# Kernel tuning notes

Hardware: AMD Instinct MI355X
Metric: run time of the kernel (lower is better)

## Reference

```python
import jax, jax.numpy as jnp
import numpy as np

N_NODES = 50000
N_EDGES = 800000
C_IN = 128
C_OUT = 128
K = 6


def setup_inputs() -> dict:
    key = jax.random.key(0)
    ks = jax.random.split(key, 8)
    nodes = jax.random.normal(ks[0], (N_NODES, C_IN), dtype=jnp.float32)
    edges = jax.random.uniform(ks[1], (N_EDGES,), dtype=jnp.float32)
    senders = jax.random.randint(ks[2], (N_EDGES,), 0, N_NODES, dtype=jnp.int32)
    receivers = jax.random.randint(ks[3], (N_EDGES,), 0, N_NODES, dtype=jnp.int32)
    # K independent Dense(out_channels) layers (kernel + bias each), plus extra module bias
    W = jax.random.normal(ks[4], (K, C_IN, C_OUT), dtype=jnp.float32) / jnp.sqrt(jnp.float32(C_IN))
    b_dense = jax.random.normal(ks[5], (K, C_OUT), dtype=jnp.float32) * 0.01
    bias = jnp.zeros((C_OUT,), dtype=jnp.float32)
    return {"nodes": nodes, "edges": edges, "senders": senders, "receivers": receivers,
            "W": W, "b_dense": b_dense, "bias": bias}


def reference(nodes, edges, senders, receivers, W, b_dense, bias):
    n = nodes.shape[0]
    # Laplacian L = D - A with A[s, r] = w. deg_i = sum of weights of edges with sender i.
    deg = jax.ops.segment_sum(edges, senders, num_segments=n)
    # lambda_max = 2 * max(L.data) where L.data = concat(deg, -edges)
    lambda_max = 2.0 * jnp.maximum(deg.max(), (-edges).max())
    scale = 2.0 / lambda_max  # L_hat = (2/lambda_max) * L

    def Lmatvec(x):  # (2L/lambda_max) @ x via gather + segment_sum
        agg = jax.ops.segment_sum(edges[:, None] * x[receivers], senders, num_segments=n)
        return scale * (deg[:, None] * x - agg)

    Tx0 = nodes
    out = Tx0 @ W[0] + b_dense[0]
    Tx1 = Lmatvec(Tx0)
    out = out + Tx1 @ W[1] + b_dense[1]
    for k in range(2, K):
        Tx2 = 2.0 * Lmatvec(Tx1) - Tx0
        out = out + Tx2 @ W[k] + b_dense[k]
        Tx0, Tx1 = Tx1, Tx2
    return out + bias
```

## Files before the change

kernel.cpp:

```cpp
#include <hip/hip_runtime.h>

#define C 128
#define KORD 6
#define KD (KORD * C)
#define EPB 2048

typedef __attribute__((ext_vector_type(8))) short short8;
typedef __attribute__((ext_vector_type(4))) float f32x4;

__device__ __forceinline__ short f2bf(float f) {
  unsigned u = __float_as_uint(f);
  unsigned r = (u + 0x7fffu + ((u >> 16) & 1u)) >> 16;
  return (short)r;
}
__device__ __forceinline__ float bf2f(short s) {
  return __uint_as_float(((unsigned)(unsigned short)s) << 16);
}

__device__ __forceinline__ unsigned enc_f32(float f) {
  unsigned u = __float_as_uint(f);
  return (u & 0x80000000u) ? ~u : (u | 0x80000000u);
}
__device__ __forceinline__ float dec_f32(unsigned u) {
  return (u & 0x80000000u) ? __uint_as_float(u ^ 0x80000000u) : __uint_as_float(~u);
}

__global__ void prep_kernel(const float* __restrict__ W, const float* __restrict__ bd,
                            const float* __restrict__ bias, short* __restrict__ Wt,
                            float* __restrict__ bsum, const float* __restrict__ nodes,
                            short* __restrict__ xb, int n) {
  int i = blockIdx.x * blockDim.x + threadIdx.x;
  if (i < KD * C) {
    int k = i >> 7, nn = i & 127;
    Wt[(size_t)nn * KD + k] = f2bf(W[i]);
  }
  if (i < C) {
    float s = bias[i];
#pragma unroll
    for (int k = 0; k < KORD; ++k) s += bd[k * C + i];
    bsum[i] = s;
  }
  if (i < n * 32) {
    int row = i >> 5, c4 = i & 31;
    float4 v = ((const float4*)nodes)[(size_t)row * 32 + c4];
    short4 o;
    o.x = f2bf(v.x); o.y = f2bf(v.y); o.z = f2bf(v.z); o.w = f2bf(v.w);
    ((short4*)(xb + (size_t)row * KD))[c4] = o;
  }
}

__global__ __launch_bounds__(256) void p1_count_kernel(const int* __restrict__ senders,
                                                       const float* __restrict__ edges, int ne,
                                                       int* __restrict__ hist, int NB,
                                                       unsigned* __restrict__ umax) {
  __shared__ int h[256];
  int t = threadIdx.x;
  h[t] = 0;
  __syncthreads();
  int base = blockIdx.x * EPB;
  int end = min(base + EPB, ne);
  float m = -INFINITY;
  for (int i = base + t; i < end; i += 256) {
    atomicAdd(&h[senders[i] >> 8], 1);
    m = fmaxf(m, -edges[i]);
  }
#pragma unroll
  for (int off = 32; off > 0; off >>= 1) m = fmaxf(m, __shfl_down(m, off, 64));
  if ((t & 63) == 0) atomicMax(umax, enc_f32(m));
  __syncthreads();
  hist[t * NB + blockIdx.x] = h[t];
}

__global__ __launch_bounds__(1024) void scan1_kernel(const int* __restrict__ counts,
                                                     int* __restrict__ offsets,
                                                     int* __restrict__ bsums, int n) {
  int t = threadIdx.x;
  int i = blockIdx.x * 1024 + t;
  int lane = t & 63, w = t >> 6;
  int v = (i < n) ? counts[i] : 0;
  int s = v;
#pragma unroll
  for (int d = 1; d < 64; d <<= 1) {
    int o = __shfl_up(s, d, 64);
    if (lane >= d) s += o;
  }
  __shared__ int wsum[16];
  if (lane == 63) wsum[w] = s;
  __syncthreads();
  if (t < 16) {
    int ws = wsum[t];
#pragma unroll
    for (int d = 1; d < 16; d <<= 1) {
      int o = __shfl_up(ws, d, 64);
      if (t >= d) ws += o;
    }
    wsum[t] = ws;
  }
  __syncthreads();
  int excl = s - v + (w > 0 ? wsum[w - 1] : 0);
  if (i < n) offsets[i] = excl;
  if (t == 1023) bsums[blockIdx.x] = wsum[15];
}

__global__ __launch_bounds__(1024) void scan2_kernel(int* __restrict__ bsums, int nb) {
  int t = threadIdx.x;
  int lane = t & 63, w = t >> 6;
  int v = (t < nb) ? bsums[t] : 0;
  int s = v;
#pragma unroll
  for (int d = 1; d < 64; d <<= 1) {
    int o = __shfl_up(s, d, 64);
    if (lane >= d) s += o;
  }
  __shared__ int wsum[16];
  if (lane == 63) wsum[w] = s;
  __syncthreads();
  if (t < 16) {
    int ws = wsum[t];
#pragma unroll
    for (int d = 1; d < 16; d <<= 1) {
      int o = __shfl_up(ws, d, 64);
      if (t >= d) ws += o;
    }
    wsum[t] = ws;
  }
  __syncthreads();
  int excl = s - v + (w > 0 ? wsum[w - 1] : 0);
  if (t < nb) bsums[t] = excl;
}

__global__ __launch_bounds__(256) void p1_scatter_kernel(
    const int* __restrict__ senders, const int* __restrict__ receivers,
    const float* __restrict__ edges, int ne, const int* __restrict__ scanned,
    const int* __restrict__ bsums, int NB, int2* __restrict__ bkt) {
  __shared__ int basec[256];
  int t = threadIdx.x;
  int idx = t * NB + blockIdx.x;
  basec[t] = scanned[idx] + bsums[idx >> 10];
  __syncthreads();
  int base = blockIdx.x * EPB;
  int end = min(base + EPB, ne);
  for (int i = base + t; i < end; i += 256) {
    int s = senders[i];
    int pos = atomicAdd(&basec[s >> 8], 1);
    int2 rec;
    rec.x = __float_as_int(edges[i]);
    rec.y = receivers[i] | ((s & 255) << 16);
    bkt[pos] = rec;
  }
}

__global__ __launch_bounds__(256) void p2_finalize_kernel(
    const int2* __restrict__ bkt, const int* __restrict__ scanned,
    const int* __restrict__ bsums, int NB, int NBUCK, int ne, int n, int2* __restrict__ csr_wr,
    int* __restrict__ offsets, float* __restrict__ degf, unsigned* __restrict__ umax,
    int* __restrict__ ticket, float* __restrict__ scalep) {
  __shared__ int h[256];
  __shared__ int cur[256];
  __shared__ float dg[256];
  __shared__ int wsum[4];
  __shared__ float wmax[4];
  int t = threadIdx.x;
  int b = blockIdx.x;
  int i0 = b * NB;
  int base = scanned[i0] + bsums[i0 >> 10];
  int bend = ne;
  if (b != NBUCK - 1) {
    int i1 = (b + 1) * NB;
    bend = scanned[i1] + bsums[i1 >> 10];
  }
  h[t] = 0;
  dg[t] = 0.f;
  __syncthreads();
  for (int i = base + t; i < bend; i += 256) atomicAdd(&h[(bkt[i].y >> 16) & 255], 1);
  __syncthreads();
  int lane = t & 63, w = t >> 6;
  int v = h[t];
  int s = v;
#pragma unroll
  for (int d = 1; d < 64; d <<= 1) {
    int o = __shfl_up(s, d, 64);
    if (lane >= d) s += o;
  }
  if (lane == 63) wsum[w] = s;
  __syncthreads();
  int carry = 0;
#pragma unroll
  for (int j = 0; j < 4; ++j) carry += (j < w) ? wsum[j] : 0;
  int excl = s - v + carry;
  int node = b * 256 + t;
  if (node < n) offsets[node] = base + excl;
  cur[t] = base + excl;
  __syncthreads();
  for (int i = base + t; i < bend; i += 256) {
    int2 rec = bkt[i];
    int bin = (rec.y >> 16) & 255;
    int pos = atomicAdd(&cur[bin], 1);
    int2 outrec;
    outrec.x = rec.x;
    outrec.y = (rec.y & 0xFFFF) * KD;
    csr_wr[pos] = outrec;
    atomicAdd(&dg[bin], __int_as_float(rec.x));
  }
  __syncthreads();
  float d = dg[t];
  if (node < n) degf[node] = d;
  float m = (node < n) ? d : 0.f;
#pragma unroll
  for (int off = 32; off > 0; off >>= 1) m = fmaxf(m, __shfl_down(m, off, 64));
  if (lane == 0) wmax[w] = m;
  __syncthreads();
  if (t == 0) {
    float mm = fmaxf(fmaxf(wmax[0], wmax[1]), fmaxf(wmax[2], wmax[3]));
    atomicMax(umax, enc_f32(mm));
    if (b == NBUCK - 1) offsets[n] = ne;
    __threadfence();
    int done = atomicAdd(ticket, 1);
    if (done == NBUCK - 1) {
      unsigned cu = atomicMax(umax, 0u);
      scalep[0] = 1.0f / dec_f32(cu);
    }
  }
}

__global__ __launch_bounds__(256, 8) void matvec_kernel(
    const short* __restrict__ xg,
    const short* __restrict__ zg,
    short* __restrict__ yg,
    const float* __restrict__ deg, const int* __restrict__ offsets,
    const int2* __restrict__ csr_wr, const float* __restrict__ scalep, float coef, int n) {
  int wid = (blockIdx.x * blockDim.x + threadIdx.x) >> 6;
  int lane = threadIdx.x & 63;
  int hw = lane >> 5;
  int qq = (lane >> 4) & 1;
  int sub = lane & 15;
  if (2 * wid >= n) return;
  int node = 2 * wid + hw;
  int nd = min(node, n - 1);
  float sc = scalep[0] * coef;
  int e0 = offsets[nd], e1 = offsets[nd + 1];
  float d = 0.f;
  short8 xo, zv;
  if (qq == 0) {
    d = deg[nd];
    xo = *(const short8*)(xg + (size_t)nd * KD + sub * 8);
    if (zg) zv = *(const short8*)(zg + (size_t)nd * KD + sub * 8);
  }
  float a[8];
#pragma unroll
  for (int j = 0; j < 8; ++j) a[j] = 0.f;
  int elast = e1 - 1;
  const short* xs = xg + sub * 8;
  for (int e = e0 + qq * 4; e < e1; e += 8) {
    int2 p0 = csr_wr[e];
    int2 p1 = csr_wr[min(e + 1, elast)];
    int2 p2 = csr_wr[min(e + 2, elast)];
    int2 p3 = csr_wr[min(e + 3, elast)];
    short8 v0 = *(const short8*)(xs + p0.y);
    short8 v1 = *(const short8*)(xs + p1.y);
    short8 v2 = *(const short8*)(xs + p2.y);
    short8 v3 = *(const short8*)(xs + p3.y);
    float w0 = __int_as_float(p0.x);
    float w1 = (e + 1 < e1) ? __int_as_float(p1.x) : 0.f;
    float w2 = (e + 2 < e1) ? __int_as_float(p2.x) : 0.f;
    float w3 = (e + 3 < e1) ? __int_as_float(p3.x) : 0.f;
#pragma unroll
    for (int j = 0; j < 8; ++j) {
      float t0 = fmaf(w0, bf2f(v0[j]), a[j]);
      float t1 = fmaf(w1, bf2f(v1[j]), t0);
      float t2 = fmaf(w2, bf2f(v2[j]), t1);
      a[j] = fmaf(w3, bf2f(v3[j]), t2);
    }
  }
#pragma unroll
  for (int j = 0; j < 8; ++j) a[j] += __shfl_xor(a[j], 16, 64);
  if (qq == 0 && node < n) {
    float r[8];
#pragma unroll
    for (int j = 0; j < 8; ++j) r[j] = sc * fmaf(d, bf2f(xo[j]), -a[j]);
    if (zg) {
#pragma unroll
      for (int j = 0; j < 8; ++j) r[j] -= bf2f(zv[j]);
    }
    short8 o;
#pragma unroll
    for (int j = 0; j < 8; ++j) o[j] = f2bf(r[j]);
    *(short8*)(yg + (size_t)nd * KD + sub * 8) = o;
  }
}

#define BK 64
#define LDP (BK + 8)
__global__ __launch_bounds__(256) void mfma_gemm_kernel(const short* __restrict__ Xb,
                                                        const short* __restrict__ Wt,
                                                        const float* __restrict__ bsum,
                                                        float* __restrict__ out, int n) {
  __shared__ short Al[64 * LDP];
  __shared__ short Bl[128 * LDP];
  int t = threadIdx.x;
  int w = t >> 6, lane = t & 63;
  int m = lane & 15, q = lane >> 4;
  int row0 = blockIdx.x * 64;
  int c0 = w * 32;

  f32x4 acc[4][2];
#pragma unroll
  for (int i = 0; i < 4; ++i)
#pragma unroll
    for (int j = 0; j < 2; ++j) acc[i][j] = (f32x4){0.f, 0.f, 0.f, 0.f};

  for (int k0 = 0; k0 < KD; k0 += BK) {
    __syncthreads();
#pragma unroll
    for (int p = 0; p < 2; ++p) {
      int idx = t + 256 * p;
      int r = idx >> 3, u = idx & 7;
      int gr = min(row0 + r, n - 1);
      short8 v = *(const short8*)(Xb + (size_t)gr * KD + k0 + u * 8);
      *(short8*)(Al + r * LDP + u * 8) = v;
    }
#pragma unroll
    for (int p = 0; p < 4; ++p) {
      int idx = t + 256 * p;
      int cc = idx >> 3, u = idx & 7;
      short8 v = *(const short8*)(Wt + (size_t)cc * KD + k0 + u * 8);
      *(short8*)(Bl + cc * LDP + u * 8) = v;
    }
    __syncthreads();
#pragma unroll
    for (int s = 0; s < 2; ++s) {
      int ko = s * 32 + q * 8;
      short8 b0 = *(const short8*)(Bl + (c0 + m) * LDP + ko);
      short8 b1 = *(const short8*)(Bl + (c0 + 16 + m) * LDP + ko);
#pragma unroll
      for (int rt = 0; rt < 4; ++rt) {
        short8 av = *(const short8*)(Al + (rt * 16 + m) * LDP + ko);
        acc[rt][0] = __builtin_amdgcn_mfma_f32_16x16x32_bf16(av, b0, acc[rt][0], 0, 0, 0);
        acc[rt][1] = __builtin_amdgcn_mfma_f32_16x16x32_bf16(av, b1, acc[rt][1], 0, 0, 0);
      }
    }
  }

#pragma unroll
  for (int ct = 0; ct < 2; ++ct) {
    int col = c0 + ct * 16 + m;
    float bs = bsum[col];
#pragma unroll
    for (int rt = 0; rt < 4; ++rt) {
#pragma unroll
      for (int i = 0; i < 4; ++i) {
        int row = row0 + rt * 16 + q * 4 + i;
        if (row < n) out[(size_t)row * C + col] = acc[rt][ct][i] + bs;
      }
    }
  }
}

extern "C" void kernel_launch(void* const* d_in, const int* in_sizes, int n_in,
                              void* d_out, int out_size, void* d_ws, size_t ws_size,
                              hipStream_t stream) {
  const float* nodes = (const float*)d_in[0];
  const float* edges = (const float*)d_in[1];
  const int* senders = (const int*)d_in[2];
  const int* receivers = (const int*)d_in[3];
  const float* W = (const float*)d_in[4];
  const float* b_dense = (const float*)d_in[5];
  const float* bias = (const float*)d_in[6];
  float* out = (float*)d_out;
  int n = in_sizes[0] / C;
  int ne = in_sizes[1];
  int NB = (ne + EPB - 1) / EPB;
  int NBUCK = (n + 255) >> 8;
  int M = 256 * NB;
  int nb2 = (M + 1023) / 1024;

  char* ws = (char*)d_ws;
  size_t off = 0;
  auto alloc = [&](size_t b) { size_t r = off; off += (b + 255) & ~(size_t)255; return r; };
  float* degf = (float*)(ws + alloc((size_t)n * 4));
  int* offsets = (int*)(ws + alloc((size_t)(n + 1) * 4));
  int* hist = (int*)(ws + alloc((size_t)M * 4));
  int* bsums = (int*)(ws + alloc((size_t)nb2 * 4));
  int2* bkt = (int2*)(ws + alloc((size_t)ne * 8));
  int2* csr_wr = (int2*)(ws + alloc((size_t)ne * 8));
  unsigned* umax = (unsigned*)(ws + alloc(8));
  float* scalep = (float*)(ws + alloc(4));
  float* bsum = (float*)(ws + alloc(C * 4));
  short* Xb = (short*)(ws + alloc((size_t)n * KD * 2));
  short* Wt = (short*)(ws + alloc((size_t)KD * C * 2));
  (void)ws_size; (void)n_in; (void)out_size;

  hipMemsetAsync(umax, 0, 8, stream);

  int prep_n = max(KD * C, n * 32);
  prep_kernel<<<(prep_n + 255) / 256, 256, 0, stream>>>(W, b_dense, bias, Wt, bsum, nodes, Xb, n);

  p1_count_kernel<<<NB, 256, 0, stream>>>(senders, edges, ne, hist, NB, umax);
  scan1_kernel<<<nb2, 1024, 0, stream>>>(hist, hist, bsums, M);
  scan2_kernel<<<1, 1024, 0, stream>>>(bsums, nb2);
  p1_scatter_kernel<<<NB, 256, 0, stream>>>(senders, receivers, edges, ne, hist, bsums, NB, bkt);
  p2_finalize_kernel<<<NBUCK, 256, 0, stream>>>(bkt, hist, bsums, NB, NBUCK, ne, n, csr_wr,
                                                offsets, degf, umax, (int*)(umax + 1), scalep);

  int mvblocks = (n * 32 + 255) / 256;

  matvec_kernel<<<mvblocks, 256, 0, stream>>>(Xb + 0 * C, nullptr, Xb + 1 * C,
                                              degf, offsets, csr_wr, scalep, 1.0f, n);
  matvec_kernel<<<mvblocks, 256, 0, stream>>>(Xb + 1 * C, Xb + 0 * C, Xb + 2 * C,
                                              degf, offsets, csr_wr, scalep, 2.0f, n);
  matvec_kernel<<<mvblocks, 256, 0, stream>>>(Xb + 2 * C, Xb + 1 * C, Xb + 3 * C,
                                              degf, offsets, csr_wr, scalep, 2.0f, n);
  matvec_kernel<<<mvblocks, 256, 0, stream>>>(Xb + 3 * C, Xb + 2 * C, Xb + 4 * C,
                                              degf, offsets, csr_wr, scalep, 2.0f, n);
  matvec_kernel<<<mvblocks, 256, 0, stream>>>(Xb + 4 * C, Xb + 3 * C, Xb + 5 * C,
                                              degf, offsets, csr_wr, scalep, 2.0f, n);

  mfma_gemm_kernel<<<(n + 63) / 64, 256, 0, stream>>>(Xb, Wt, bsum, out, n);
}
```

Before: 344.4 us.

## Split SpMV channels across grid passes with one wave per node

Restructures the Laplacian matvec so each wave handles one node and only a 32-channel slice of the features, with a second grid dimension of four passes covering all channels. Each lane group reads 64-byte slices of 16 edges in parallel, then reduces across lanes with shuffles. The aim is more independent gathers in flight per node and a smaller working set per pass that may stay in cache. In exchange the CSR indices and weights are reread four times, and the cross-lane reduction plus the 1024-thread blocks add overhead.

```diff
diff --git a/kernel.cpp b/kernel.cpp
--- a/kernel.cpp
+++ b/kernel.cpp
@@ -4,6 +4,7 @@
 #define KORD 6
 #define KD (KORD * C)
 #define EPB 2048
+#define NPASS 4
 
 typedef __attribute__((ext_vector_type(8))) short short8;
 typedef __attribute__((ext_vector_type(4))) float f32x4;
@@ -223,58 +224,55 @@
   }
 }
 
-__global__ __launch_bounds__(256, 8) void matvec_kernel(
+__global__ __launch_bounds__(1024, 8) void matvec_kernel(
     const short* __restrict__ xg,
     const short* __restrict__ zg,
     short* __restrict__ yg,
     const float* __restrict__ deg, const int* __restrict__ offsets,
     const int2* __restrict__ csr_wr, const float* __restrict__ scalep, float coef, int n) {
-  int wid = (blockIdx.x * blockDim.x + threadIdx.x) >> 6;
+  int wave = threadIdx.x >> 6;
+  int node = blockIdx.x * 16 + wave;
+  if (node >= n) return;
   int lane = threadIdx.x & 63;
-  int hw = lane >> 5;
-  int qq = (lane >> 4) & 1;
-  int sub = lane & 15;
-  if (2 * wid >= n) return;
-  int node = 2 * wid + hw;
-  int nd = min(node, n - 1);
+  int g = lane >> 2;
+  int sl = lane & 3;
+  int co = blockIdx.y * 32 + sl * 8;
   float sc = scalep[0] * coef;
-  int e0 = offsets[nd], e1 = offsets[nd + 1];
+  int e0 = offsets[node], e1 = offsets[node + 1];
   float d = 0.f;
   short8 xo, zv;
-  if (qq == 0) {
-    d = deg[nd];
-    xo = *(const short8*)(xg + (size_t)nd * KD + sub * 8);
-    if (zg) zv = *(const short8*)(zg + (size_t)nd * KD + sub * 8);
+  if (g == 0) {
+    d = deg[node];
+    xo = *(const short8*)(xg + (size_t)node * KD + co);
+    if (zg) zv = *(const short8*)(zg + (size_t)node * KD + co);
   }
   float a[8];
 #pragma unroll
   for (int j = 0; j < 8; ++j) a[j] = 0.f;
+  const short* xs = xg + co;
   int elast = e1 - 1;
-  const short* xs = xg + sub * 8;
-  for (int e = e0 + qq * 4; e < e1; e += 8) {
+  for (int e = e0 + g; e < e1; e += 32) {
+    int e2 = e + 16;
     int2 p0 = csr_wr[e];
-    int2 p1 = csr_wr[min(e + 1, elast)];
-    int2 p2 = csr_wr[min(e + 2, elast)];
-    int2 p3 = csr_wr[min(e + 3, elast)];
+    int2 p1 = csr_wr[min(e2, elast)];
     short8 v0 = *(const short8*)(xs + p0.y);
     short8 v1 = *(const short8*)(xs + p1.y);
-    short8 v2 = *(const short8*)(xs + p2.y);
-    short8 v3 = *(const short8*)(xs + p3.y);
     float w0 = __int_as_float(p0.x);
-    float w1 = (e + 1 < e1) ? __int_as_float(p1.x) : 0.f;
-    float w2 = (e + 2 < e1) ? __int_as_float(p2.x) : 0.f;
-    float w3 = (e + 3 < e1) ? __int_as_float(p3.x) : 0.f;
+    float w1 = (e2 < e1) ? __int_as_float(p1.x) : 0.f;
 #pragma unroll
     for (int j = 0; j < 8; ++j) {
       float t0 = fmaf(w0, bf2f(v0[j]), a[j]);
-      float t1 = fmaf(w1, bf2f(v1[j]), t0);
-      float t2 = fmaf(w2, bf2f(v2[j]), t1);
-      a[j] = fmaf(w3, bf2f(v3[j]), t2);
-    }
-  }
-#pragma unroll
-  for (int j = 0; j < 8; ++j) a[j] += __shfl_xor(a[j], 16, 64);
-  if (qq == 0 && node < n) {
+      a[j] = fmaf(w1, bf2f(v1[j]), t0);
+    }
+  }
+#pragma unroll
+  for (int j = 0; j < 8; ++j) {
+    a[j] += __shfl_xor(a[j], 4, 64);
+    a[j] += __shfl_xor(a[j], 8, 64);
+    a[j] += __shfl_xor(a[j], 16, 64);
+    a[j] += __shfl_xor(a[j], 32, 64);
+  }
+  if (g == 0) {
     float r[8];
 #pragma unroll
     for (int j = 0; j < 8; ++j) r[j] = sc * fmaf(d, bf2f(xo[j]), -a[j]);
@@ -285,7 +283,7 @@
     short8 o;
 #pragma unroll
     for (int j = 0; j < 8; ++j) o[j] = f2bf(r[j]);
-    *(short8*)(yg + (size_t)nd * KD + sub * 8) = o;
+    *(short8*)(yg + (size_t)node * KD + co) = o;
   }
 }
 
@@ -402,18 +400,18 @@
   p2_finalize_kernel<<<NBUCK, 256, 0, stream>>>(bkt, hist, bsums, NB, NBUCK, ne, n, csr_wr,
                                                 offsets, degf, umax, (int*)(umax + 1), scalep);
 
-  int mvblocks = (n * 32 + 255) / 256;
-
-  matvec_kernel<<<mvblocks, 256, 0, stream>>>(Xb + 0 * C, nullptr, Xb + 1 * C,
-                                              degf, offsets, csr_wr, scalep, 1.0f, n);
-  matvec_kernel<<<mvblocks, 256, 0, stream>>>(Xb + 1 * C, Xb + 0 * C, Xb + 2 * C,
-                                              degf, offsets, csr_wr, scalep, 2.0f, n);
-  matvec_kernel<<<mvblocks, 256, 0, stream>>>(Xb + 2 * C, Xb + 1 * C, Xb + 3 * C,
-                                              degf, offsets, csr_wr, scalep, 2.0f, n);
-  matvec_kernel<<<mvblocks, 256, 0, stream>>>(Xb + 3 * C, Xb + 2 * C, Xb + 4 * C,
-                                              degf, offsets, csr_wr, scalep, 2.0f, n);
-  matvec_kernel<<<mvblocks, 256, 0, stream>>>(Xb + 4 * C, Xb + 3 * C, Xb + 5 * C,
-                                              degf, offsets, csr_wr, scalep, 2.0f, n);
+  dim3 mvgrid((n + 15) / 16, NPASS);
+
+  matvec_kernel<<<mvgrid, 1024, 0, stream>>>(Xb + 0 * C, nullptr, Xb + 1 * C,
+                                             degf, offsets, csr_wr, scalep, 1.0f, n);
+  matvec_kernel<<<mvgrid, 1024, 0, stream>>>(Xb + 1 * C, Xb + 0 * C, Xb + 2 * C,
+                                             degf, offsets, csr_wr, scalep, 2.0f, n);
+  matvec_kernel<<<mvgrid, 1024, 0, stream>>>(Xb + 2 * C, Xb + 1 * C, Xb + 3 * C,
+                                             degf, offsets, csr_wr, scalep, 2.0f, n);
+  matvec_kernel<<<mvgrid, 1024, 0, stream>>>(Xb + 3 * C, Xb + 2 * C, Xb + 4 * C,
+                                             degf, offsets, csr_wr, scalep, 2.0f, n);
+  matvec_kernel<<<mvgrid, 1024, 0, stream>>>(Xb + 4 * C, Xb + 3 * C, Xb + 5 * C,
+                                             degf, offsets, csr_wr, scalep, 2.0f, n);
 
   mfma_gemm_kernel<<<(n + 63) / 64, 256, 0, stream>>>(Xb, Wt, bsum, out, n);
 }
```

Measured after the change: 580.4 us. 68.5% more time.
